# Kernel tuning notes

Hardware: AMD Instinct MI355X
Metric: run time of the kernel (lower is better)

Reference implementation:

```python
import jax, jax.numpy as jnp
import numpy as np

EMBED, HEADS, LEVELS, POINTS = 256, 8, 3, 4
SPATIAL = np.array([[128, 128], [64, 64], [32, 32]], dtype=np.int64)  # (H, W) per level
B = 2
S = int((SPATIAL[:, 0] * SPATIAL[:, 1]).sum())  # 21504
Q = S  # encoder self-attention: queries == flattened multi-scale features


def grid_sample_bilinear(img, grid):
    """img: [N,C,H,W]; grid: [N,Q,P,2] (x,y) in [-1,1]; bilinear, zeros padding, align_corners=False.
    Returns [N,C,Q,P]."""
    N, C, H, W = img.shape
    _, Qn, Pn, _ = grid.shape
    x = (grid[..., 0] + 1.0) * (W * 0.5) - 0.5
    y = (grid[..., 1] + 1.0) * (H * 0.5) - 0.5
    x0 = jnp.floor(x)
    y0 = jnp.floor(y)
    wx1 = x - x0
    wy1 = y - y0
    x0i = x0.astype(jnp.int32)
    y0i = y0.astype(jnp.int32)
    imgf = img.reshape(N, C, H * W)

    def gather(ix, iy):
        valid = (ix >= 0) & (ix < W) & (iy >= 0) & (iy < H)
        ixc = jnp.clip(ix, 0, W - 1)
        iyc = jnp.clip(iy, 0, H - 1)
        flat = (iyc * W + ixc).reshape(N, -1)  # [N, Q*P]
        v = jax.vmap(lambda im, f: im[:, f])(imgf, flat)  # [N, C, Q*P]
        return jnp.where(valid.reshape(N, 1, -1), v, 0.0)

    w00 = ((1.0 - wx1) * (1.0 - wy1)).reshape(N, 1, -1)
    w01 = (wx1 * (1.0 - wy1)).reshape(N, 1, -1)
    w10 = ((1.0 - wx1) * wy1).reshape(N, 1, -1)
    w11 = (wx1 * wy1).reshape(N, 1, -1)
    out = (gather(x0i, y0i) * w00 + gather(x0i + 1, y0i) * w01
           + gather(x0i, y0i + 1) * w10 + gather(x0i + 1, y0i + 1) * w11)
    return out.reshape(N, C, Qn, Pn)


def msda_forward(hidden_states, encoder_hidden_states, reference_points, shapes_np,
                 sampling_offsets_w, sampling_offsets_b, attention_weights_w, attention_weights_b,
                 value_proj_w, value_proj_b, output_proj_w, output_proj_b):
    Bn, Qn, E = hidden_states.shape
    H, L, P = HEADS, LEVELS, POINTS
    D = E // H
    Sn = encoder_hidden_states.shape[1]
    value = (encoder_hidden_states @ value_proj_w.T + value_proj_b).reshape(Bn, Sn, H, D)
    off = (hidden_states @ sampling_offsets_w.T + sampling_offsets_b).reshape(Bn, Qn, H, L, P, 2)
    aw = hidden_states @ attention_weights_w.T + attention_weights_b
    aw = jax.nn.softmax(aw.reshape(Bn, Qn, H, L * P), axis=-1).reshape(Bn, Qn, H, L, P)
    # offset normalizer is (W, H) per level
    norm = jnp.asarray(np.stack([shapes_np[:, 1], shapes_np[:, 0]], axis=-1), dtype=hidden_states.dtype)
    loc = reference_points[:, :, None, :, None, :] + off / norm[None, None, None, :, None, :]
    grids = 2.0 * loc - 1.0  # [B,Q,H,L,P,2]
    out = jnp.zeros((Bn * H, D, Qn), value.dtype)
    start = 0
    for lvl in range(L):  # small static loop over levels (distinct spatial shapes)
        h, w = int(shapes_np[lvl, 0]), int(shapes_np[lvl, 1])
        val_l = value[:, start:start + h * w].transpose(0, 2, 3, 1).reshape(Bn * H, D, h, w)
        start += h * w
        g = grids[:, :, :, lvl].transpose(0, 2, 1, 3, 4).reshape(Bn * H, Qn, P, 2)
        sampled = grid_sample_bilinear(val_l, g)  # [B*H, D, Q, P]
        w_l = aw[:, :, :, lvl].transpose(0, 2, 1, 3).reshape(Bn * H, 1, Qn, P)
        out = out + (sampled * w_l).sum(-1)
    out = out.reshape(Bn, H * D, Qn).transpose(0, 2, 1)  # [B,Q,E]
    return out @ output_proj_w.T + output_proj_b


def setup_inputs():
    key = jax.random.key(0)
    ks = jax.random.split(key, 11)
    sc = 0.02
    E, H, L, P = EMBED, HEADS, LEVELS, POINTS
    return {
        "hidden_states": jax.random.normal(ks[0], (B, Q, E), jnp.float32),
        "encoder_hidden_states": jax.random.normal(ks[1], (B, S, E), jnp.float32),
        "reference_points": jax.random.uniform(ks[2], (B, Q, L, 2), jnp.float32),
        "spatial_shapes": jnp.asarray(SPATIAL),
        "sampling_offsets_w": jax.random.normal(ks[3], (H * L * P * 2, E), jnp.float32) * sc,
        "sampling_offsets_b": jax.random.normal(ks[4], (H * L * P * 2,), jnp.float32) * sc,
        "attention_weights_w": jax.random.normal(ks[5], (H * L * P, E), jnp.float32) * sc,
        "attention_weights_b": jax.random.normal(ks[6], (H * L * P,), jnp.float32) * sc,
        "value_proj_w": jax.random.normal(ks[7], (E, E), jnp.float32) * sc,
        "value_proj_b": jax.random.normal(ks[8], (E,), jnp.float32) * sc,
        "output_proj_w": jax.random.normal(ks[9], (E, E), jnp.float32) * sc,
        "output_proj_b": jax.random.normal(ks[10], (E,), jnp.float32) * sc,
    }


def reference(hidden_states, encoder_hidden_states, reference_points, spatial_shapes,
              sampling_offsets_w, sampling_offsets_b, attention_weights_w, attention_weights_b,
              value_proj_w, value_proj_b, output_proj_w, output_proj_b):
    shapes_np = np.asarray(spatial_shapes)  # static per-level (H, W)
    return msda_forward(hidden_states, encoder_hidden_states, reference_points, shapes_np,
                        sampling_offsets_w, sampling_offsets_b, attention_weights_w, attention_weights_b,
                        value_proj_w, value_proj_b, output_proj_w, output_proj_b)
```

## Files before the change

kernel.cpp:

```cpp
#include <hip/hip_runtime.h>
#include <hip/hip_bf16.h>

#define EMBED   256
#define HEADS   8
#define LEVELS  3
#define POINTS  4
#define BATCH   2
#define QLEN    21504
#define SLEN    21504
#define MTOT    (BATCH * QLEN)

typedef __attribute__((ext_vector_type(8))) short short8;
typedef __attribute__((ext_vector_type(4))) float f32x4;
typedef __attribute__((ext_vector_type(2))) float f32x2;

__device__ __forceinline__ short f2bf(float x) {
    unsigned u = __builtin_bit_cast(unsigned, x);
    u += 0x7fffu + ((u >> 16) & 1u);
    return (short)(u >> 16);
}
__device__ __forceinline__ f32x2 bfpair(unsigned u) {
    f32x2 r;
    r.x = __builtin_bit_cast(float, u << 16);
    r.y = __builtin_bit_cast(float, u & 0xffff0000u);
    return r;
}
__device__ __forceinline__ void async16(const void* g, void* l) {
    __builtin_amdgcn_global_load_lds((const __attribute__((address_space(1))) void*)g,
                                     (__attribute__((address_space(3))) void*)l, 16, 0, 0);
}

__global__ __launch_bounds__(256)
void pack_weights_kernel(const float* __restrict__ vW, const float* __restrict__ oW,
                         const float* __restrict__ soW, const float* __restrict__ awW,
                         const float* __restrict__ soB, const float* __restrict__ awB,
                         short* __restrict__ vWb, short* __restrict__ oWb,
                         short* __restrict__ soawWb, float* __restrict__ soawB)
{
    int i = blockIdx.x * 256 + threadIdx.x;
    if (i < 65536) {
        vWb[i] = f2bf(vW[i]);
    } else if (i < 131072) {
        int j = i - 65536;
        oWb[j] = f2bf(oW[j]);
    } else if (i < 204800) {
        int j = i - 131072;
        int row = j >> 8, k = j & 255;
        float v = (row < 192) ? soW[row * 256 + k] : awW[(row - 192) * 256 + k];
        soawWb[j] = f2bf(v);
    } else if (i < 205088) {
        int row = i - 204800;
        soawB[row] = (row < 192) ? soB[row] : awB[row - 192];
    }
}


__global__ __launch_bounds__(512, 4)
void proj_gemm_kernel(const float* __restrict__ enc, const short* __restrict__ vWb,
                      const float* __restrict__ vB, short* __restrict__ valb,
                      const float* __restrict__ hs, const short* __restrict__ soawWb,
                      const float* __restrict__ soawB, float* __restrict__ offaw)
{
    __shared__ short Ws[128 * 256];
    const int tid  = threadIdx.x;
    const int lane = tid & 63, wv = tid >> 6;
    const int m16  = lane & 15, ko = lane >> 4;
    const int bx   = blockIdx.x;
    const bool isVal   = (bx < 2);
    const int  colbase = isVal ? bx * 128 : (bx - 2) * 96;
    const int  gcols   = isVal ? 128 : 96;
    const short* Wt    = isVal ? vWb : soawWb;
    const float* A     = isVal ? enc : hs;
    const float* bias  = isVal ? vB  : soawB;

    const int nch = gcols * 32;
    for (int c = tid; c < nch; c += 512) {
        const int colL = c >> 5;
        const int cw   = c & 31;
        const int csw  = (cw & 24) | ((cw ^ colL) & 7);
        async16(Wt + (((size_t)(colbase + colL)) << 8) + csw * 8, Ws + c * 8);
    }

    const int strip = blockIdx.y * 256 + wv * 32;
    short8 afr[2][8];
    #pragma unroll
    for (int rt = 0; rt < 2; ++rt) {
        const float* Af = A + (size_t)(strip + rt * 16 + m16) * 256 + ko * 8;
        #pragma unroll
        for (int kt = 0; kt < 8; ++kt) {
            float4 x = *(const float4*)(Af + kt * 32);
            float4 y = *(const float4*)(Af + kt * 32 + 4);
            short8 t;
            t[0] = f2bf(x.x); t[1] = f2bf(x.y); t[2] = f2bf(x.z); t[3] = f2bf(x.w);
            t[4] = f2bf(y.x); t[5] = f2bf(y.y); t[6] = f2bf(y.z); t[7] = f2bf(y.w);
            afr[rt][kt] = t;
        }
    }
    __syncthreads();

    const short8* Wvp = (const short8*)Ws;
    const int r0  = strip + ko * 4;
    const int nct = gcols >> 4;
    for (int ct = 0; ct < nct; ++ct) {
        const int colL = ct * 16 + m16;
        f32x4 a0 = (f32x4)0.f;
        f32x4 a1 = (f32x4)0.f;
        #pragma unroll
        for (int kt = 0; kt < 8; ++kt) {
            const int g = kt * 4 + ko;
            const int s = (g & 24) | ((g ^ colL) & 7);
            const short8 bfrag = Wvp[colL * 32 + s];
            a0 = __builtin_amdgcn_mfma_f32_16x16x32_bf16(afr[0][kt], bfrag, a0, 0, 0, 0);
            a1 = __builtin_amdgcn_mfma_f32_16x16x32_bf16(afr[1][kt], bfrag, a1, 0, 0, 0);
        }
        const int col = colbase + colL;
        const float bv = bias[col];
        if (isVal) {
            const int hh = col >> 5, ch = col & 31;
            #pragma unroll
            for (int rt = 0; rt < 2; ++rt) {
                const f32x4 a = rt ? a1 : a0;
                #pragma unroll
                for (int r = 0; r < 4; ++r) {
                    const int rg = r0 + rt * 16 + r;
                    const int b  = (rg >= SLEN) ? 1 : 0;
                    const int sx = rg - b * SLEN;
                    valb[(((size_t)(b * 8 + hh)) * SLEN + sx) * 32 + ch] = f2bf(a[r] + bv);
                }
            }
        } else {
            #pragma unroll
            for (int rt = 0; rt < 2; ++rt) {
                const f32x4 a = rt ? a1 : a0;
                #pragma unroll
                for (int r = 0; r < 4; ++r)
                    offaw[(size_t)(r0 + rt * 16 + r) * 288 + col] = a[r] + bv;
            }
        }
    }
}

__global__ __launch_bounds__(512, 4)
void out_gemm_kernel(const short* __restrict__ A, const short* __restrict__ oWb,
                     const float* __restrict__ oB, float* __restrict__ C)
{
    __shared__ short Ws[128 * 256];
    const int tid  = threadIdx.x;
    const int lane = tid & 63, wv = tid >> 6;
    const int m16  = lane & 15, ko = lane >> 4;
    const int colbase = blockIdx.x * 128;

    for (int c = tid; c < 4096; c += 512) {
        const int colL = c >> 5;
        const int cw   = c & 31;
        const int csw  = (cw & 24) | ((cw ^ colL) & 7);
        async16(oWb + (((size_t)(colbase + colL)) << 8) + csw * 8, Ws + c * 8);
    }

    const int strip = blockIdx.y * 256 + wv * 32;
    short8 afr[2][8];
    #pragma unroll
    for (int rt = 0; rt < 2; ++rt) {
        const short* Ab = A + (size_t)(strip + rt * 16 + m16) * 256 + ko * 8;
        #pragma unroll
        for (int kt = 0; kt < 8; ++kt) afr[rt][kt] = *(const short8*)(Ab + kt * 32);
    }
    __syncthreads();

    const short8* Wvp = (const short8*)Ws;
    const int r0 = strip + ko * 4;
    for (int ct = 0; ct < 8; ++ct) {
        const int colL = ct * 16 + m16;
        f32x4 a0 = (f32x4)0.f;
        f32x4 a1 = (f32x4)0.f;
        #pragma unroll
        for (int kt = 0; kt < 8; ++kt) {
            const int g = kt * 4 + ko;
            const int s = (g & 24) | ((g ^ colL) & 7);
            const short8 bfrag = Wvp[colL * 32 + s];
            a0 = __builtin_amdgcn_mfma_f32_16x16x32_bf16(afr[0][kt], bfrag, a0, 0, 0, 0);
            a1 = __builtin_amdgcn_mfma_f32_16x16x32_bf16(afr[1][kt], bfrag, a1, 0, 0, 0);
        }
        const int col = colbase + colL;
        const float bv = oB[col];
        #pragma unroll
        for (int rt = 0; rt < 2; ++rt) {
            const f32x4 a = rt ? a1 : a0;
            #pragma unroll
            for (int r = 0; r < 4; ++r)
                C[(size_t)(r0 + rt * 16 + r) * 256 + col] = a[r] + bv;
        }
    }
}

__global__ __launch_bounds__(256, 8)
void msda_sample_kernel(const short* __restrict__ value,
                        const float* __restrict__ offaw,
                        const float* __restrict__ ref,
                        short* __restrict__ attn)
{
    __shared__ int prep[32 * 76];

    const int tid = threadIdx.x;
    const int g   = tid >> 3;
    const int sub = tid & 7;
    const int t   = sub >> 2;

    const int blk = blockIdx.x;
    const int h   = blk & 7;
    const int j   = blk >> 3;
    const int b   = (j >= 672) ? 1 : 0;
    const int qc  = j - b * 672;
    const int q   = qc * 32 + g;
    const int bq  = b * QLEN + q;

    {
        const float* awp = offaw + (size_t)bq * 288 + 192 + h * 12;
        const float4 wa = *(const float4*)(awp);
        const float4 wb = *(const float4*)(awp + 4);
        const float4 wc = *(const float4*)(awp + 8);
        float w[12] = { wa.x, wa.y, wa.z, wa.w, wb.x, wb.y, wb.z, wb.w,
                        wc.x, wc.y, wc.z, wc.w };
        float mx = w[0];
        #pragma unroll
        for (int i = 1; i < 12; ++i) mx = fmaxf(mx, w[i]);
        float s = 0.f;
        #pragma unroll
        for (int i = 0; i < 12; ++i) s += __expf(w[i] - mx);
        const float inv = 1.f / s;

        const float* offp = offaw + (size_t)bq * 288 + h * 24;
        const float* refp = ref + (size_t)bq * 6;
        const int npts = (sub < 4) ? 2 : 1;
        #pragma unroll
        for (int it = 0; it < 2; ++it) {
            if (it >= npts) break;
            const int p  = sub + it * 8;
            const int l  = p >> 2;
            const int Wl = 128 >> l;
            const int st = (l == 0) ? 0 : (l == 1 ? 16384 : 20480);

            const float2 oxy = *(const float2*)(offp + p * 2);
            const float2 rxy = *(const float2*)(refp + 2 * l);
            const float ox = oxy.x, oy = oxy.y;
            const float rx = rxy.x, ry = rxy.y;
            const float a  = __expf(w[p] - mx) * inv;

            const float x = fmaf(rx, (float)Wl, ox - 0.5f);
            const float y = fmaf(ry, (float)Wl, oy - 0.5f);
            const float x0f = floorf(x), y0f = floorf(y);
            const int   x0  = (int)x0f,  y0  = (int)y0f;
            const float wx1 = x - x0f, wy1 = y - y0f;
            const float wx0 = 1.f - wx1, wy0 = 1.f - wy1;
            const bool vy0 = (unsigned)y0       < (unsigned)Wl;
            const bool vy1 = (unsigned)(y0 + 1) < (unsigned)Wl;

            const int xs = min(max(x0, 0), Wl - 2);
            const float wl0 = (xs == x0) ? wx0 : ((xs == x0 + 1) ? wx1 : 0.f);
            const float wl1 = (xs == x0) ? wx1 : ((xs + 1 == x0) ? wx0 : 0.f);

            const int hb = (b * 8 + h) * SLEN + st;
            const int o0 = vy0 ? (hb + y0 * Wl + xs) * 64       : 0;
            const int o1 = vy1 ? (hb + (y0 + 1) * Wl + xs) * 64 : 0;

            int* pp = &prep[g * 76 + p * 6];
            pp[0] = o0;
            pp[1] = o1;
            pp[2] = __builtin_bit_cast(int, vy0 ? wy0 * wl0 * a : 0.f);
            pp[3] = __builtin_bit_cast(int, vy0 ? wy0 * wl1 * a : 0.f);
            pp[4] = __builtin_bit_cast(int, vy1 ? wy1 * wl0 * a : 0.f);
            pp[5] = __builtin_bit_cast(int, vy1 ? wy1 * wl1 * a : 0.f);
        }
    }
    __syncthreads();

    const char* vbytes = (const char*)value;
    const unsigned subb = (unsigned)sub * 16u;
    f32x2 acc2[4];
    acc2[0] = (f32x2)0.f; acc2[1] = (f32x2)0.f;
    acc2[2] = (f32x2)0.f; acc2[3] = (f32x2)0.f;

    #pragma unroll
    for (int pb = 0; pb < 4; ++pb) {
        int4  v[6];
        float wgt[6];
        #pragma unroll
        for (int i = 0; i < 3; ++i) {
            const int p = pb * 3 + i;
            const int* pp = &prep[g * 76 + p * 6];
            const unsigned o0 = (unsigned)pp[0] + subb;
            const unsigned o1 = (unsigned)pp[1] + subb;
            wgt[2*i]   = __builtin_bit_cast(float, pp[2 + t]);
            wgt[2*i+1] = __builtin_bit_cast(float, pp[4 + t]);
            v[2*i]   = *(const int4*)(vbytes + (size_t)o0);
            v[2*i+1] = *(const int4*)(vbytes + (size_t)o1);
        }
        #pragma unroll
        for (int i = 0; i < 6; ++i) {
            f32x2 w2; w2.x = wgt[i]; w2.y = wgt[i];
            acc2[0] = __builtin_elementwise_fma(w2, bfpair((unsigned)v[i].x), acc2[0]);
            acc2[1] = __builtin_elementwise_fma(w2, bfpair((unsigned)v[i].y), acc2[1]);
            acc2[2] = __builtin_elementwise_fma(w2, bfpair((unsigned)v[i].z), acc2[2]);
            acc2[3] = __builtin_elementwise_fma(w2, bfpair((unsigned)v[i].w), acc2[3]);
        }
    }

    #pragma unroll
    for (int j2 = 0; j2 < 4; ++j2) {
        acc2[j2].x += __shfl_xor(acc2[j2].x, 4);
        acc2[j2].y += __shfl_xor(acc2[j2].y, 4);
    }

    if (sub < 4) {
        int4 o;
        o.x = ((unsigned)(unsigned short)f2bf(acc2[0].y) << 16) | (unsigned short)f2bf(acc2[0].x);
        o.y = ((unsigned)(unsigned short)f2bf(acc2[1].y) << 16) | (unsigned short)f2bf(acc2[1].x);
        o.z = ((unsigned)(unsigned short)f2bf(acc2[2].y) << 16) | (unsigned short)f2bf(acc2[2].x);
        o.w = ((unsigned)(unsigned short)f2bf(acc2[3].y) << 16) | (unsigned short)f2bf(acc2[3].x);
        ((int4*)attn)[(size_t)bq * 32 + h * 4 + sub] = o;
    }
}

extern "C" void kernel_launch(void* const* d_in, const int* in_sizes, int n_in,
                              void* d_out, int out_size, void* d_ws, size_t ws_size,
                              hipStream_t stream) {
    const float* hs  = (const float*)d_in[0];
    const float* enc = (const float*)d_in[1];
    const float* rp  = (const float*)d_in[2];
    const float* soW = (const float*)d_in[4];
    const float* soB = (const float*)d_in[5];
    const float* awW = (const float*)d_in[6];
    const float* awB = (const float*)d_in[7];
    const float* vW  = (const float*)d_in[8];
    const float* vB  = (const float*)d_in[9];
    const float* oW  = (const float*)d_in[10];
    const float* oB  = (const float*)d_in[11];
    float* out = (float*)d_out;

    const int M = MTOT;
    const size_t ME = (size_t)M * 256;

    short* valb   = (short*)d_ws;
    short* attnb  = valb + ME;
    float* offaw  = (float*)(attnb + ME);
    short* vWb    = (short*)(offaw + (size_t)M * 288);
    short* oWb    = vWb + 65536;
    short* soawWb = oWb + 65536;
    float* soawB  = (float*)(soawWb + 73728);

    pack_weights_kernel<<<dim3(802), dim3(256), 0, stream>>>(vW, oW, soW, awW, soB, awB,
                                                             vWb, oWb, soawWb, soawB);
    proj_gemm_kernel<<<dim3(5, 168), dim3(512), 0, stream>>>(enc, vWb, vB, valb,
                                                             hs, soawWb, soawB, offaw);
    msda_sample_kernel<<<dim3(M / 4), dim3(256), 0, stream>>>(valb, offaw, rp, attnb);
    out_gemm_kernel<<<dim3(2, 168), dim3(512), 0, stream>>>(attnb, oWb, oB, out);
}
```

Measured before the change: 267.2 us.

## Pre-pack weights into MFMA fragment order and read B from global, drop LDS staging

The weight pack kernel now writes bf16 weights in per-lane MFMA B-fragment order, so the GEMM kernels read each fragment with one coalesced 16-byte global load instead of staging through swizzled LDS. Each GEMM block now covers all output columns for a 128-row strip with 256 threads. This removes the LDS fill, the barrier and the redundant A-fragment loads and conversions across column blocks. In exchange, every wave streams the whole weight matrix from L2/global on every block, which depends on cache hit rates.

```diff
diff --git a/kernel.cpp b/kernel.cpp
--- a/kernel.cpp
+++ b/kernel.cpp
@@ -25,63 +25,52 @@
     r.y = __builtin_bit_cast(float, u & 0xffff0000u);
     return r;
 }
-__device__ __forceinline__ void async16(const void* g, void* l) {
-    __builtin_amdgcn_global_load_lds((const __attribute__((address_space(1))) void*)g,
-                                     (__attribute__((address_space(3))) void*)l, 16, 0, 0);
-}
 
 __global__ __launch_bounds__(256)
 void pack_weights_kernel(const float* __restrict__ vW, const float* __restrict__ oW,
                          const float* __restrict__ soW, const float* __restrict__ awW,
                          const float* __restrict__ soB, const float* __restrict__ awB,
-                         short* __restrict__ vWb, short* __restrict__ oWb,
-                         short* __restrict__ soawWb, float* __restrict__ soawB)
+                         short* __restrict__ vWf, short* __restrict__ oWf,
+                         short* __restrict__ soawWf, float* __restrict__ soawB)
 {
     int i = blockIdx.x * 256 + threadIdx.x;
-    if (i < 65536) {
-        vWb[i] = f2bf(vW[i]);
-    } else if (i < 131072) {
-        int j = i - 65536;
-        oWb[j] = f2bf(oW[j]);
-    } else if (i < 204800) {
-        int j = i - 131072;
-        int row = j >> 8, k = j & 255;
-        float v = (row < 192) ? soW[row * 256 + k] : awW[(row - 192) * 256 + k];
-        soawWb[j] = f2bf(v);
-    } else if (i < 205088) {
-        int row = i - 204800;
+    if (i < 25600) {
+        const float* src; short* dst; int rem;
+        if (i < 8192)       { src = vW; dst = vWf; rem = i; }
+        else if (i < 16384) { src = oW; dst = oWf; rem = i - 8192; }
+        else                { src = nullptr; dst = soawWf; rem = i - 16384; }
+        const int lane = rem & 63;
+        const int kt   = (rem >> 6) & 7;
+        const int ct   = rem >> 9;
+        const int col  = ct * 16 + (lane & 15);
+        const int kb   = (kt * 4 + (lane >> 4)) * 8;
+        const float* p = src ? (src + col * 256 + kb)
+                             : ((col < 192) ? (soW + col * 256 + kb)
+                                            : (awW + (col - 192) * 256 + kb));
+        short8 t;
+        #pragma unroll
+        for (int j = 0; j < 8; ++j) t[j] = f2bf(p[j]);
+        *(short8*)(dst + (size_t)rem * 8) = t;
+    } else if (i < 25888) {
+        int row = i - 25600;
         soawB[row] = (row < 192) ? soB[row] : awB[row - 192];
     }
 }
 
 
-__global__ __launch_bounds__(512, 4)
-void proj_gemm_kernel(const float* __restrict__ enc, const short* __restrict__ vWb,
+__global__ __launch_bounds__(256, 2)
+void proj_gemm_kernel(const float* __restrict__ enc, const short* __restrict__ vWf,
                       const float* __restrict__ vB, short* __restrict__ valb,
-                      const float* __restrict__ hs, const short* __restrict__ soawWb,
+                      const float* __restrict__ hs, const short* __restrict__ soawWf,
                       const float* __restrict__ soawB, float* __restrict__ offaw)
 {
-    __shared__ short Ws[128 * 256];
     const int tid  = threadIdx.x;
     const int lane = tid & 63, wv = tid >> 6;
     const int m16  = lane & 15, ko = lane >> 4;
-    const int bx   = blockIdx.x;
-    const bool isVal   = (bx < 2);
-    const int  colbase = isVal ? bx * 128 : (bx - 2) * 96;
-    const int  gcols   = isVal ? 128 : 96;
-    const short* Wt    = isVal ? vWb : soawWb;
-    const float* A     = isVal ? enc : hs;
-    const float* bias  = isVal ? vB  : soawB;
-
-    const int nch = gcols * 32;
-    for (int c = tid; c < nch; c += 512) {
-        const int colL = c >> 5;
-        const int cw   = c & 31;
-        const int csw  = (cw & 24) | ((cw ^ colL) & 7);
-        async16(Wt + (((size_t)(colbase + colL)) << 8) + csw * 8, Ws + c * 8);
-    }
-
-    const int strip = blockIdx.y * 256 + wv * 32;
+    const bool isVal = (blockIdx.x == 0);
+    const float* A   = isVal ? enc : hs;
+    const int strip  = blockIdx.y * 128 + wv * 32;
+
     short8 afr[2][8];
     #pragma unroll
     for (int rt = 0; rt < 2; ++rt) {
@@ -96,24 +85,22 @@
             afr[rt][kt] = t;
         }
     }
-    __syncthreads();
-
-    const short8* Wvp = (const short8*)Ws;
-    const int r0  = strip + ko * 4;
-    const int nct = gcols >> 4;
+
+    const short8* Wf  = (const short8*)(isVal ? vWf : soawWf);
+    const float* bias = isVal ? vB : soawB;
+    const int nct     = isVal ? 16 : 18;
+    const int r0      = strip + ko * 4;
+
     for (int ct = 0; ct < nct; ++ct) {
-        const int colL = ct * 16 + m16;
         f32x4 a0 = (f32x4)0.f;
         f32x4 a1 = (f32x4)0.f;
         #pragma unroll
         for (int kt = 0; kt < 8; ++kt) {
-            const int g = kt * 4 + ko;
-            const int s = (g & 24) | ((g ^ colL) & 7);
-            const short8 bfrag = Wvp[colL * 32 + s];
+            const short8 bfrag = Wf[(ct * 8 + kt) * 64 + lane];
             a0 = __builtin_amdgcn_mfma_f32_16x16x32_bf16(afr[0][kt], bfrag, a0, 0, 0, 0);
             a1 = __builtin_amdgcn_mfma_f32_16x16x32_bf16(afr[1][kt], bfrag, a1, 0, 0, 0);
         }
-        const int col = colbase + colL;
+        const int col = ct * 16 + m16;
         const float bv = bias[col];
         if (isVal) {
             const int hh = col >> 5, ch = col & 31;
@@ -140,24 +127,15 @@
     }
 }
 
-__global__ __launch_bounds__(512, 4)
-void out_gemm_kernel(const short* __restrict__ A, const short* __restrict__ oWb,
+__global__ __launch_bounds__(256, 2)
+void out_gemm_kernel(const short* __restrict__ A, const short* __restrict__ oWf,
                      const float* __restrict__ oB, float* __restrict__ C)
 {
-    __shared__ short Ws[128 * 256];
     const int tid  = threadIdx.x;
     const int lane = tid & 63, wv = tid >> 6;
     const int m16  = lane & 15, ko = lane >> 4;
-    const int colbase = blockIdx.x * 128;
-
-    for (int c = tid; c < 4096; c += 512) {
-        const int colL = c >> 5;
-        const int cw   = c & 31;
-        const int csw  = (cw & 24) | ((cw ^ colL) & 7);
-        async16(oWb + (((size_t)(colbase + colL)) << 8) + csw * 8, Ws + c * 8);
-    }
-
-    const int strip = blockIdx.y * 256 + wv * 32;
+    const int strip = blockIdx.x * 128 + wv * 32;
+
     short8 afr[2][8];
     #pragma unroll
     for (int rt = 0; rt < 2; ++rt) {
@@ -165,23 +143,19 @@
         #pragma unroll
         for (int kt = 0; kt < 8; ++kt) afr[rt][kt] = *(const short8*)(Ab + kt * 32);
     }
-    __syncthreads();
-
-    const short8* Wvp = (const short8*)Ws;
+
+    const short8* Wf = (const short8*)oWf;
     const int r0 = strip + ko * 4;
-    for (int ct = 0; ct < 8; ++ct) {
-        const int colL = ct * 16 + m16;
+    for (int ct = 0; ct < 16; ++ct) {
         f32x4 a0 = (f32x4)0.f;
         f32x4 a1 = (f32x4)0.f;
         #pragma unroll
         for (int kt = 0; kt < 8; ++kt) {
-            const int g = kt * 4 + ko;
-            const int s = (g & 24) | ((g ^ colL) & 7);
-            const short8 bfrag = Wvp[colL * 32 + s];
+            const short8 bfrag = Wf[(ct * 8 + kt) * 64 + lane];
             a0 = __builtin_amdgcn_mfma_f32_16x16x32_bf16(afr[0][kt], bfrag, a0, 0, 0, 0);
             a1 = __builtin_amdgcn_mfma_f32_16x16x32_bf16(afr[1][kt], bfrag, a1, 0, 0, 0);
         }
-        const int col = colbase + colL;
+        const int col = ct * 16 + m16;
         const float bv = oB[col];
         #pragma unroll
         for (int rt = 0; rt < 2; ++rt) {
@@ -343,15 +317,15 @@
     short* valb   = (short*)d_ws;
     short* attnb  = valb + ME;
     float* offaw  = (float*)(attnb + ME);
-    short* vWb    = (short*)(offaw + (size_t)M * 288);
-    short* oWb    = vWb + 65536;
-    short* soawWb = oWb + 65536;
-    float* soawB  = (float*)(soawWb + 73728);
-
-    pack_weights_kernel<<<dim3(802), dim3(256), 0, stream>>>(vW, oW, soW, awW, soB, awB,
-                                                             vWb, oWb, soawWb, soawB);
-    proj_gemm_kernel<<<dim3(5, 168), dim3(512), 0, stream>>>(enc, vWb, vB, valb,
-                                                             hs, soawWb, soawB, offaw);
+    short* vWf    = (short*)(offaw + (size_t)M * 288);
+    short* oWf    = vWf + 65536;
+    short* soawWf = oWf + 65536;
+    float* soawB  = (float*)(soawWf + 73728);
+
+    pack_weights_kernel<<<dim3(102), dim3(256), 0, stream>>>(vW, oW, soW, awW, soB, awB,
+                                                             vWf, oWf, soawWf, soawB);
+    proj_gemm_kernel<<<dim3(2, 336), dim3(256), 0, stream>>>(enc, vWf, vB, valb,
+                                                             hs, soawWf, soawB, offaw);
     msda_sample_kernel<<<dim3(M / 4), dim3(256), 0, stream>>>(valb, offaw, rp, attnb);
-    out_gemm_kernel<<<dim3(2, 168), dim3(512), 0, stream>>>(attnb, oWb, oB, out);
-}
+    out_gemm_kernel<<<dim3(336), dim3(256), 0, stream>>>(attnb, oWf, oB, out);
+}
```

After: 249.2 us. -6.7%, faster.
